# Kernel optimization log

Measured on AMD Instinct MI355X. Metric: run time of the kernel, lower is better.

Reference implementation:

```python
import jax, jax.numpy as jnp
import numpy as np
import math

N_HEADS = 16  # matches init_kwargs n_heads


def setup_inputs() -> dict:
    key = jax.random.key(0)
    k1, k2, k3 = jax.random.split(key, 3)
    B, S, D = 8, 1024, 1024
    x = jax.random.normal(k1, (B, S, D), dtype=jnp.float32)
    Wc = jax.random.normal(k2, (D, 3 * D), dtype=jnp.float32) * 0.02
    bc = jnp.zeros((3 * D,), dtype=jnp.float32)
    Wo = jax.random.normal(k3, (D, D), dtype=jnp.float32) * 0.02
    bo = jnp.zeros((D,), dtype=jnp.float32)
    return {"x": x, "Wc": Wc, "bc": bc, "Wo": Wo, "bo": bo}


def reference(x, Wc, bc, Wo, bo):
    B, S, D = x.shape
    H = N_HEADS
    hd = D // H
    qkv = x @ Wc + bc                         # [B,S,3D]
    q, k, v = jnp.split(qkv, 3, axis=2)
    q = q.reshape(B, S, H, hd)
    k = k.reshape(B, S, H, hd)
    v = v.reshape(B, S, H, hd)
    # NOTE: source scales by sqrt(d_size), not sqrt(head_dim)
    scores = jnp.einsum("bqhd,bkhd->bhqk", q, k) / math.sqrt(D)
    # source mask: triu(ones) kept, zeros (k < q) filled with float32 min
    # i.e. attend only to positions k >= q (anti-causal, faithful to source)
    keep = jnp.triu(jnp.ones((S, S), dtype=bool))  # [S,S]
    neg = jnp.finfo(jnp.float32).min
    scores = jnp.where(keep[None, None, :, :], scores, neg)
    attn = jax.nn.softmax(scores, axis=-1)    # [B,H,S,S]; dropout p=0 -> identity
    out = jnp.einsum("bhqk,bkhd->bqhd", attn, v)
    concat = out.reshape(B, S, D)
    return concat @ Wo + bo                   # final dropout p=0 -> identity
```

## Files before the change

### kernel.cpp

```cpp
#include <hip/hip_runtime.h>
#include <stdint.h>

typedef __attribute__((ext_vector_type(8))) short  bf16x8;
typedef __attribute__((ext_vector_type(4))) short  short4v;
typedef __attribute__((ext_vector_type(4))) float  f32x4;
typedef __attribute__((ext_vector_type(4))) float  float4v;

#define VMW(N) asm volatile("s_waitcnt vmcnt(" #N ")" ::: "memory")
#define BAR()  asm volatile("s_barrier" ::: "memory")

__device__ __forceinline__ short f2bf(float f) {
  union { float f; uint32_t u; } c; c.f = f;
  uint32_t u = c.u;
  uint32_t r = (u + 0x7FFFu + ((u >> 16) & 1u)) >> 16;
  return (short)(uint16_t)r;
}

__device__ __forceinline__ short f2bf_hw(float f) {
  return __builtin_bit_cast(short, (__bf16)f);
}

__device__ __forceinline__ void gload_lds16(const void* g, void* l) {
  __builtin_amdgcn_global_load_lds(
      (const __attribute__((address_space(1))) void*)g,
      (__attribute__((address_space(3))) void*)l, 16, 0, 0);
}

__device__ __forceinline__ void transpose_body(
    const float* __restrict__ in, short* __restrict__ out, int R, int C,
    int bx, int by, short (*tile)[65]) {
  int bc = bx * 64, br = by * 64;
  int tc = threadIdx.x & 63, tr = threadIdx.x >> 6;
#pragma unroll
  for (int i = 0; i < 64; i += 4)
    tile[tc][tr + i] = f2bf(in[(size_t)(br + tr + i) * C + bc + tc]);
  __syncthreads();
#pragma unroll
  for (int i = 0; i < 64; i += 4)
    out[(size_t)(bc + tr + i) * R + br + tc] = tile[tr + i][tc];
}

__global__ __launch_bounds__(256) void k_prep(
    const float* __restrict__ x, short* __restrict__ xb, int n4,
    const float* __restrict__ Wc, short* __restrict__ wct,
    const float* __restrict__ Wo, short* __restrict__ wot) {
  __shared__ short tile[64][65];
  const int id = blockIdx.x;
  if (id < 1024) {
    const int stride = 1024 * 256;
    for (int i = id * 256 + threadIdx.x; i < n4; i += stride) {
      float4v v = *(const float4v*)(x + (size_t)i * 4);
      short4v o;
      o.x = f2bf(v.x); o.y = f2bf(v.y); o.z = f2bf(v.z); o.w = f2bf(v.w);
      *(short4v*)(xb + (size_t)i * 4) = o;
    }
  } else if (id < 1024 + 768) {
    int t = id - 1024;
    transpose_body(Wc, wct, 1024, 3072, t % 48, t / 48, tile);
  } else {
    int t = id - 1792;
    transpose_body(Wo, wot, 1024, 1024, t & 15, t >> 4, tile);
  }
}

template <bool F32OUT>
__global__ __launch_bounds__(256) void k_gemm2(
    const short* __restrict__ A, const short* __restrict__ BT,
    const float* __restrict__ bias, void* __restrict__ Cout,
    int M, int N, int K, int nbn) {
  __shared__ short SM[2][2][2][128][32];
  const int tid = threadIdx.x;
  const int w = tid >> 6, l = tid & 63;
  const int fr = l & 15, fg = l >> 4;
  const int wm = w >> 1, wn = w & 1;

  const int q8 = gridDim.x >> 3;
  const int wg = (blockIdx.x & 7) * q8 + (blockIdx.x >> 3);
  const int bm = wg / nbn, bn = wg % nbn;
  const size_t brow = (size_t)bm << 7;
  const int bcol = bn << 7;

  const int NT = K >> 6;

  const int srow = l >> 2;
  const int soct = (l & 3) ^ ((l >> 3) & 3);
  const short* aG = A + (brow + srow) * (size_t)K + soct * 8;
  const short* bG = BT + ((size_t)(bcol + srow)) * K + soct * 8;
  const int slot8 = ((fg ^ ((fr >> 1) & 3)) << 3);

  f32x4 acc[4][4] = {};

#pragma unroll
  for (int s = 0; s < 6; ++s) {
    const int t = s >> 2, tau = s & 3, buf = t & 1, mat = tau & 1, kh = tau >> 1;
    const int kbase = t * 64 + kh * 32;
    const short* g0 = (mat ? bG : aG) + kbase;
#pragma unroll
    for (int j = 0; j < 2; ++j) {
      const int r0 = (w * 2 + j) * 16;
      gload_lds16(g0 + (size_t)r0 * K, (char*)&SM[buf][mat][kh][r0][0]);
    }
  }
  VMW(8);
  BAR();

  int sidx = 6;
  for (int t = 0; t < NT; ++t) {
    const int buf = t & 1;
#pragma unroll
    for (int p = 0; p < 2; ++p) {
      const int kh = p;
#pragma unroll
      for (int s = 0; s < 2; ++s) {
        if (sidx < NT * 4) {
          const int ts = sidx >> 2, tau = sidx & 3;
          const int sb = ts & 1, mat = tau & 1, skh = tau >> 1;
          const int kbase = ts * 64 + skh * 32;
          const short* g0 = (mat ? bG : aG) + kbase;
#pragma unroll
          for (int j = 0; j < 2; ++j) {
            const int r0 = (w * 2 + j) * 16;
            gload_lds16(g0 + (size_t)r0 * K, (char*)&SM[sb][mat][skh][r0][0]);
          }
          ++sidx;
        }
      }
      bf16x8 af[4], bf[4];
#pragma unroll
      for (int m = 0; m < 4; ++m)
        af[m] = *(const bf16x8*)&SM[buf][0][kh][wm * 64 + m * 16 + fr][slot8];
#pragma unroll
      for (int n = 0; n < 4; ++n)
        bf[n] = *(const bf16x8*)&SM[buf][1][kh][wn * 64 + n * 16 + fr][slot8];
      BAR();
      __builtin_amdgcn_s_setprio(1);
#pragma unroll
      for (int m = 0; m < 4; ++m)
#pragma unroll
        for (int n = 0; n < 4; ++n)
          acc[m][n] = __builtin_amdgcn_mfma_f32_16x16x32_bf16(
              af[m], bf[n], acc[m][n], 0, 0, 0);
      __builtin_amdgcn_s_setprio(0);
      if (!(t == NT - 1 && p == 1)) {
        if (t == NT - 1 && p == 0) { VMW(0); }
        else if (t == NT - 2 && p == 1) { VMW(4); }
        else { VMW(8); }
        BAR();
      }
    }
  }

#pragma unroll
  for (int n = 0; n < 4; ++n) {
    const int col = bcol + wn * 64 + n * 16 + fr;
    const float bv = bias[col];
#pragma unroll
    for (int i = 0; i < 4; ++i) {
      const size_t row = brow + (size_t)(wm * 64 + i * 16 + fg * 4);
#pragma unroll
      for (int r = 0; r < 4; ++r) {
        const float v = acc[i][n][r] + bv;
        if (F32OUT)
          ((float*)Cout)[(row + r) * (size_t)N + col] = v;
        else
          ((short*)Cout)[(row + r) * (size_t)N + col] = f2bf(v);
      }
    }
  }
}

__global__ __launch_bounds__(256) void k_attn(
    const short* __restrict__ qkv, short* __restrict__ outc, int Bn, int S) {
  __shared__ short Ks[128][64];
  __shared__ short Vt[64][136];

  const int tid = threadIdx.x;
  const int w = tid >> 6, l = tid & 63;
  const int fr = l & 15, fg = l >> 4;

  const int tq = blockIdx.x >> 7;
  const int bh = blockIdx.x & 127;
  const int h = bh & 15, b = bh >> 4;
  const int q0 = tq << 6;

  const size_t rowbase = (size_t)b * S;
  const int qcol = q0 + w * 16 + fr;

  bf16x8 qf[2];
  {
    const short* qp = qkv + (rowbase + qcol) * 3072 + h * 64 + fg * 8;
    qf[0] = *(const bf16x8*)qp;
    qf[1] = *(const bf16x8*)(qp + 32);
    const float C2 = 0.04508422f;
#pragma unroll
    for (int j = 0; j < 8; ++j) {
      union { float f; uint32_t u; } ca, cb;
      ca.u = ((uint32_t)(uint16_t)qf[0][j]) << 16;
      cb.u = ((uint32_t)(uint16_t)qf[1][j]) << 16;
      qf[0][j] = f2bf_hw(ca.f * C2);
      qf[1][j] = f2bf_hw(cb.f * C2);
    }
  }

  f32x4 o[4] = {};
  float lacc = 0.0f;

  const short* Kbase = qkv + rowbase * 3072 + 1024 + h * 64;
  const short* Vbase = qkv + rowbase * 3072 + 2048 + h * 64;

  const int r8 = l >> 3, slot = l & 7;
  const int vdb = (tid >> 4) << 2;

#define STAGE_K(c)                                                             \
  {                                                                            \
    const int k0s = (c) << 7;                                                  \
    _Pragma("unroll") for (int j = 0; j < 4; ++j) {                            \
      int ch = w * 4 + j;                                                      \
      int row = ch * 8 + r8;                                                   \
      int d = (slot ^ (row & 7)) << 3;                                         \
      gload_lds16(Kbase + (size_t)(k0s + row) * 3072 + d,                      \
                  (char*)&Ks[0][0] + ch * 1024);                               \
    }                                                                          \
  }
#define LOAD_V(c)                                                              \
  {                                                                            \
    const int k0s = (c) << 7;                                                  \
    _Pragma("unroll") for (int kh = 0; kh < 2; ++kh) {                         \
      int kb = ((tid & 15) << 2) + (kh << 6);                                  \
      const short* vp = Vbase + (size_t)(k0s + kb) * 3072 + vdb;               \
      vr[kh][0] = *(const short4v*)(vp);                                       \
      vr[kh][1] = *(const short4v*)(vp + 3072);                                \
      vr[kh][2] = *(const short4v*)(vp + 2 * 3072);                            \
      vr[kh][3] = *(const short4v*)(vp + 3 * 3072);                            \
    }                                                                          \
  }

  const int c0 = tq >> 1;
  short4v vr[2][4];
  STAGE_K(c0);
  LOAD_V(c0);

  for (int c = c0; c < 8; ++c) {
    const int k0 = c << 7;
    VMW(0);
    __syncthreads();

#pragma unroll
    for (int kh = 0; kh < 2; ++kh) {
      int kb = ((tid & 15) << 2) + (kh << 6);
      short4v t0 = {vr[kh][0].x, vr[kh][1].x, vr[kh][2].x, vr[kh][3].x};
      short4v t1 = {vr[kh][0].y, vr[kh][1].y, vr[kh][2].y, vr[kh][3].y};
      short4v t2 = {vr[kh][0].z, vr[kh][1].z, vr[kh][2].z, vr[kh][3].z};
      short4v t3 = {vr[kh][0].w, vr[kh][1].w, vr[kh][2].w, vr[kh][3].w};
      *(short4v*)&Vt[vdb + 0][kb] = t0;
      *(short4v*)&Vt[vdb + 1][kb] = t1;
      *(short4v*)&Vt[vdb + 2][kb] = t2;
      *(short4v*)&Vt[vdb + 3][kb] = t3;
    }

    f32x4 st[8];
#pragma unroll
    for (int kb = 0; kb < 8; ++kb) {
      f32x4 z = {0.f, 0.f, 0.f, 0.f};
      int row = kb * 16 + fr;
      int sw = row & 7;
      bf16x8 kf0 = *(const bf16x8*)&Ks[row][(fg ^ sw) << 3];
      bf16x8 kf1 = *(const bf16x8*)&Ks[row][((4 + fg) ^ sw) << 3];
      z = __builtin_amdgcn_mfma_f32_16x16x32_bf16(kf0, qf[0], z, 0, 0, 0);
      z = __builtin_amdgcn_mfma_f32_16x16x32_bf16(kf1, qf[1], z, 0, 0, 0);
      st[kb] = z;
    }

    if (c + 1 < 8) LOAD_V(c + 1);

    const bool masked = (c == c0);
#pragma unroll
    for (int kb = 0; kb < 8; ++kb)
#pragma unroll
      for (int r = 0; r < 4; ++r) {
        float e = exp2f(st[kb][r]);
        if (masked) {
          int kg = k0 + kb * 16 + fg * 4 + r;
          e = (kg < qcol) ? 0.0f : e;
        }
        st[kb][r] = e;
        lacc += e;
      }

    __syncthreads();

    if (c + 1 < 8) STAGE_K(c + 1);

#pragma unroll
    for (int kb2 = 0; kb2 < 4; ++kb2) {
      bf16x8 pa = {f2bf_hw(st[2 * kb2][0]),     f2bf_hw(st[2 * kb2][1]),
                   f2bf_hw(st[2 * kb2][2]),     f2bf_hw(st[2 * kb2][3]),
                   f2bf_hw(st[2 * kb2 + 1][0]), f2bf_hw(st[2 * kb2 + 1][1]),
                   f2bf_hw(st[2 * kb2 + 1][2]), f2bf_hw(st[2 * kb2 + 1][3])};
#pragma unroll
      for (int f = 0; f < 4; ++f) {
        short4v v0 = *(const short4v*)&Vt[f * 16 + fr][kb2 * 32 + fg * 4];
        short4v v1 = *(const short4v*)&Vt[f * 16 + fr][kb2 * 32 + 16 + fg * 4];
        bf16x8 vb = {v0.x, v0.y, v0.z, v0.w, v1.x, v1.y, v1.z, v1.w};
        o[f] = __builtin_amdgcn_mfma_f32_16x16x32_bf16(pa, vb, o[f], 0, 0, 0);
      }
    }
  }
#undef STAGE_K
#undef LOAD_V

  lacc += __shfl_xor(lacc, 16, 64);
  lacc += __shfl_xor(lacc, 32, 64);
#pragma unroll
  for (int r = 0; r < 4; ++r) {
    float denom = __shfl(lacc, fg * 4 + r, 64);
    float inv = 1.0f / denom;
    size_t orow = rowbase + (size_t)(q0 + w * 16 + fg * 4 + r);
    short* op = outc + orow * 1024 + h * 64 + fr;
#pragma unroll
    for (int f = 0; f < 4; ++f) op[f * 16] = f2bf(o[f][r] * inv);
  }
}

extern "C" void kernel_launch(void* const* d_in, const int* in_sizes, int n_in,
                              void* d_out, int out_size, void* d_ws,
                              size_t ws_size, hipStream_t stream) {
  const float* x = (const float*)d_in[0];
  const float* Wc = (const float*)d_in[1];
  const float* bc = (const float*)d_in[2];
  const float* Wo = (const float*)d_in[3];
  const float* bo = (const float*)d_in[4];
  float* out = (float*)d_out;

  const int Bn = 8, S = 1024, D = 1024;
  const int M = Bn * S;

  char* ws = (char*)d_ws;
  short* xb  = (short*)(ws);
  short* wct = (short*)(ws + (size_t)16 * 1024 * 1024);
  short* wot = (short*)(ws + (size_t)22 * 1024 * 1024);
  short* qkv = (short*)(ws + (size_t)24 * 1024 * 1024);
  short* cat = (short*)(ws + (size_t)72 * 1024 * 1024);

  k_prep<<<2048, 256, 0, stream>>>(x, xb, M * D / 4, Wc, wct, Wo, wot);
  k_gemm2<false><<<(M / 128) * (3 * D / 128), 256, 0, stream>>>(
      xb, wct, bc, qkv, M, 3 * D, D, 3 * D / 128);
  k_attn<<<16 * 128, 256, 0, stream>>>(qkv, cat, Bn, S);
  k_gemm2<true><<<(M / 128) * (D / 128), 256, 0, stream>>>(
      cat, wot, bo, out, M, D, D, D / 128);
}
```

Before: 159.0 us.

## Restructure GEMM pipeline into triple-buffered 32-wide K stages

Replaces the double-buffered 64-wide K tile loop (split into two 32-wide halves with fine-grained staged loads) with a triple-buffered ring of 32-wide K stages prefetched two steps ahead. Each iteration uses one barrier before issuing the next prefetch and computing, and shared memory drops from 4 to 3 half-tiles. This simplifies the issue schedule and sync pattern, but leaves less compute per barrier and changes how load latency overlaps with MFMA work.

```diff
diff --git a/kernel.cpp b/kernel.cpp
--- a/kernel.cpp
+++ b/kernel.cpp
@@ -68,7 +68,7 @@
     const short* __restrict__ A, const short* __restrict__ BT,
     const float* __restrict__ bias, void* __restrict__ Cout,
     int M, int N, int K, int nbn) {
-  __shared__ short SM[2][2][2][128][32];
+  __shared__ short SM[3][2][128][32];
   const int tid = threadIdx.x;
   const int w = tid >> 6, l = tid & 63;
   const int fr = l & 15, fg = l >> 4;
@@ -80,7 +80,7 @@
   const size_t brow = (size_t)bm << 7;
   const int bcol = bn << 7;
 
-  const int NT = K >> 6;
+  const int NT = K >> 5;
 
   const int srow = l >> 2;
   const int soct = (l & 3) ^ ((l >> 3) & 3);
@@ -90,65 +90,46 @@
 
   f32x4 acc[4][4] = {};
 
-#pragma unroll
-  for (int s = 0; s < 6; ++s) {
-    const int t = s >> 2, tau = s & 3, buf = t & 1, mat = tau & 1, kh = tau >> 1;
-    const int kbase = t * 64 + kh * 32;
-    const short* g0 = (mat ? bG : aG) + kbase;
-#pragma unroll
-    for (int j = 0; j < 2; ++j) {
-      const int r0 = (w * 2 + j) * 16;
-      gload_lds16(g0 + (size_t)r0 * K, (char*)&SM[buf][mat][kh][r0][0]);
-    }
-  }
-  VMW(8);
+#define STAGE_T(bufv, kt)                                                      \
+  {                                                                            \
+    _Pragma("unroll") for (int j = 0; j < 2; ++j) {                            \
+      const int r0 = (w * 2 + j) * 16;                                         \
+      gload_lds16(aG + (size_t)r0 * K + (kt)*32,                               \
+                  (char*)&SM[bufv][0][r0][0]);                                 \
+      gload_lds16(bG + (size_t)r0 * K + (kt)*32,                               \
+                  (char*)&SM[bufv][1][r0][0]);                                 \
+    }                                                                          \
+  }
+
+  STAGE_T(0, 0);
+  STAGE_T(1, 1);
+  VMW(4);
   BAR();
 
-  int sidx = 6;
   for (int t = 0; t < NT; ++t) {
-    const int buf = t & 1;
-#pragma unroll
-    for (int p = 0; p < 2; ++p) {
-      const int kh = p;
-#pragma unroll
-      for (int s = 0; s < 2; ++s) {
-        if (sidx < NT * 4) {
-          const int ts = sidx >> 2, tau = sidx & 3;
-          const int sb = ts & 1, mat = tau & 1, skh = tau >> 1;
-          const int kbase = ts * 64 + skh * 32;
-          const short* g0 = (mat ? bG : aG) + kbase;
-#pragma unroll
-          for (int j = 0; j < 2; ++j) {
-            const int r0 = (w * 2 + j) * 16;
-            gload_lds16(g0 + (size_t)r0 * K, (char*)&SM[sb][mat][skh][r0][0]);
-          }
-          ++sidx;
-        }
-      }
-      bf16x8 af[4], bf[4];
-#pragma unroll
-      for (int m = 0; m < 4; ++m)
-        af[m] = *(const bf16x8*)&SM[buf][0][kh][wm * 64 + m * 16 + fr][slot8];
+    const int buf = t % 3;
+    if (t > 0) {
+      if (t == NT - 1) { VMW(0); } else { VMW(4); }
+      BAR();
+    }
+    if (t + 2 < NT) STAGE_T((t + 2) % 3, t + 2);
+    bf16x8 af[4], bf[4];
+#pragma unroll
+    for (int m = 0; m < 4; ++m)
+      af[m] = *(const bf16x8*)&SM[buf][0][wm * 64 + m * 16 + fr][slot8];
+#pragma unroll
+    for (int n = 0; n < 4; ++n)
+      bf[n] = *(const bf16x8*)&SM[buf][1][wn * 64 + n * 16 + fr][slot8];
+    __builtin_amdgcn_s_setprio(1);
+#pragma unroll
+    for (int m = 0; m < 4; ++m)
 #pragma unroll
       for (int n = 0; n < 4; ++n)
-        bf[n] = *(const bf16x8*)&SM[buf][1][kh][wn * 64 + n * 16 + fr][slot8];
-      BAR();
-      __builtin_amdgcn_s_setprio(1);
-#pragma unroll
-      for (int m = 0; m < 4; ++m)
-#pragma unroll
-        for (int n = 0; n < 4; ++n)
-          acc[m][n] = __builtin_amdgcn_mfma_f32_16x16x32_bf16(
-              af[m], bf[n], acc[m][n], 0, 0, 0);
-      __builtin_amdgcn_s_setprio(0);
-      if (!(t == NT - 1 && p == 1)) {
-        if (t == NT - 1 && p == 0) { VMW(0); }
-        else if (t == NT - 2 && p == 1) { VMW(4); }
-        else { VMW(8); }
-        BAR();
-      }
-    }
-  }
+        acc[m][n] = __builtin_amdgcn_mfma_f32_16x16x32_bf16(
+            af[m], bf[n], acc[m][n], 0, 0, 0);
+    __builtin_amdgcn_s_setprio(0);
+  }
+#undef STAGE_T
 
 #pragma unroll
   for (int n = 0; n < 4; ++n) {
```

After: 159.7 us. About the same (+0.4%).

## Process two 64-row query tiles per attention block to reuse K/V loads

Applied to the files above, without the earlier changes.

Each attention block now handles 128 query rows (two 64-row tiles) instead of 64, so every K/V chunk staged in LDS serves twice as many queries and the grid is halved. This cuts global K/V traffic and the per-chunk staging and barrier overhead. In exchange each thread holds twice the accumulators and Q fragments, which raises register pressure and may lower occupancy. The second tile also processes the diagonal chunk, where about half of its work is masked out.

```diff
diff --git a/kernel.cpp b/kernel.cpp
--- a/kernel.cpp
+++ b/kernel.cpp
@@ -178,44 +178,54 @@
   const int w = tid >> 6, l = tid & 63;
   const int fr = l & 15, fg = l >> 4;
 
-  const int tq = blockIdx.x >> 7;
+  const int j = blockIdx.x >> 7;
   const int bh = blockIdx.x & 127;
   const int h = bh & 15, b = bh >> 4;
-  const int q0 = tq << 6;
+  const int q0a = j << 7;
+  const int q0b = q0a + 64;
 
   const size_t rowbase = (size_t)b * S;
-  const int qcol = q0 + w * 16 + fr;
-
-  bf16x8 qf[2];
+  const int qcola = q0a + w * 16 + fr;
+  const int qcolb = qcola + 64;
+
+  bf16x8 qfa[2], qfb[2];
   {
-    const short* qp = qkv + (rowbase + qcol) * 3072 + h * 64 + fg * 8;
-    qf[0] = *(const bf16x8*)qp;
-    qf[1] = *(const bf16x8*)(qp + 32);
     const float C2 = 0.04508422f;
-#pragma unroll
-    for (int j = 0; j < 8; ++j) {
-      union { float f; uint32_t u; } ca, cb;
-      ca.u = ((uint32_t)(uint16_t)qf[0][j]) << 16;
-      cb.u = ((uint32_t)(uint16_t)qf[1][j]) << 16;
-      qf[0][j] = f2bf_hw(ca.f * C2);
-      qf[1][j] = f2bf_hw(cb.f * C2);
-    }
-  }
-
-  f32x4 o[4] = {};
-  float lacc = 0.0f;
+    const short* qp = qkv + (rowbase + qcola) * 3072 + h * 64 + fg * 8;
+    const short* qq = qp + (size_t)64 * 3072;
+    qfa[0] = *(const bf16x8*)qp;  qfa[1] = *(const bf16x8*)(qp + 32);
+    qfb[0] = *(const bf16x8*)qq;  qfb[1] = *(const bf16x8*)(qq + 32);
+#pragma unroll
+    for (int i = 0; i < 8; ++i) {
+      union { float f; uint32_t u; } c0u, c1u, c2u, c3u;
+      c0u.u = ((uint32_t)(uint16_t)qfa[0][i]) << 16;
+      c1u.u = ((uint32_t)(uint16_t)qfa[1][i]) << 16;
+      c2u.u = ((uint32_t)(uint16_t)qfb[0][i]) << 16;
+      c3u.u = ((uint32_t)(uint16_t)qfb[1][i]) << 16;
+      qfa[0][i] = f2bf_hw(c0u.f * C2);
+      qfa[1][i] = f2bf_hw(c1u.f * C2);
+      qfb[0][i] = f2bf_hw(c2u.f * C2);
+      qfb[1][i] = f2bf_hw(c3u.f * C2);
+    }
+  }
+
+  f32x4 oa[4] = {}, ob[4] = {};
+  float la = 0.0f, lb = 0.0f;
 
   const short* Kbase = qkv + rowbase * 3072 + 1024 + h * 64;
   const short* Vbase = qkv + rowbase * 3072 + 2048 + h * 64;
 
   const int r8 = l >> 3, slot = l & 7;
   const int vdb = (tid >> 4) << 2;
+  const int c0 = j;
+
+  short4v vr[2][4];
 
 #define STAGE_K(c)                                                             \
   {                                                                            \
     const int k0s = (c) << 7;                                                  \
-    _Pragma("unroll") for (int j = 0; j < 4; ++j) {                            \
-      int ch = w * 4 + j;                                                      \
+    _Pragma("unroll") for (int jj = 0; jj < 4; ++jj) {                         \
+      int ch = w * 4 + jj;                                                     \
       int row = ch * 8 + r8;                                                   \
       int d = (slot ^ (row & 7)) << 3;                                         \
       gload_lds16(Kbase + (size_t)(k0s + row) * 3072 + d,                      \
@@ -235,13 +245,59 @@
     }                                                                          \
   }
 
-  const int c0 = tq >> 1;
-  short4v vr[2][4];
+  auto qksm = [&](const bf16x8* qf, int qcol, float& lac, bf16x8* pa, int c) {
+    f32x4 st[8];
+#pragma unroll
+    for (int kb = 0; kb < 8; ++kb) {
+      f32x4 z = {0.f, 0.f, 0.f, 0.f};
+      int row = kb * 16 + fr;
+      int sw = row & 7;
+      bf16x8 kf0 = *(const bf16x8*)&Ks[row][(fg ^ sw) << 3];
+      bf16x8 kf1 = *(const bf16x8*)&Ks[row][((4 + fg) ^ sw) << 3];
+      z = __builtin_amdgcn_mfma_f32_16x16x32_bf16(kf0, qf[0], z, 0, 0, 0);
+      z = __builtin_amdgcn_mfma_f32_16x16x32_bf16(kf1, qf[1], z, 0, 0, 0);
+      st[kb] = z;
+    }
+    const bool masked = (c == c0);
+    const int k0m = c << 7;
+#pragma unroll
+    for (int kb = 0; kb < 8; ++kb)
+#pragma unroll
+      for (int r = 0; r < 4; ++r) {
+        float e = exp2f(st[kb][r]);
+        if (masked) {
+          int kg = k0m + kb * 16 + fg * 4 + r;
+          e = (kg < qcol) ? 0.0f : e;
+        }
+        st[kb][r] = e;
+        lac += e;
+      }
+#pragma unroll
+    for (int kb2 = 0; kb2 < 4; ++kb2) {
+      bf16x8 t = {f2bf_hw(st[2 * kb2][0]),     f2bf_hw(st[2 * kb2][1]),
+                  f2bf_hw(st[2 * kb2][2]),     f2bf_hw(st[2 * kb2][3]),
+                  f2bf_hw(st[2 * kb2 + 1][0]), f2bf_hw(st[2 * kb2 + 1][1]),
+                  f2bf_hw(st[2 * kb2 + 1][2]), f2bf_hw(st[2 * kb2 + 1][3])};
+      pa[kb2] = t;
+    }
+  };
+  auto pv = [&](const bf16x8* pa, f32x4* o) {
+#pragma unroll
+    for (int kb2 = 0; kb2 < 4; ++kb2) {
+#pragma unroll
+      for (int f = 0; f < 4; ++f) {
+        short4v v0 = *(const short4v*)&Vt[f * 16 + fr][kb2 * 32 + fg * 4];
+        short4v v1 = *(const short4v*)&Vt[f * 16 + fr][kb2 * 32 + 16 + fg * 4];
+        bf16x8 vb = {v0.x, v0.y, v0.z, v0.w, v1.x, v1.y, v1.z, v1.w};
+        o[f] = __builtin_amdgcn_mfma_f32_16x16x32_bf16(pa[kb2], vb, o[f], 0, 0, 0);
+      }
+    }
+  };
+
   STAGE_K(c0);
   LOAD_V(c0);
 
   for (int c = c0; c < 8; ++c) {
-    const int k0 = c << 7;
     VMW(0);
     __syncthreads();
 
@@ -258,67 +314,40 @@
       *(short4v*)&Vt[vdb + 3][kb] = t3;
     }
 
-    f32x4 st[8];
-#pragma unroll
-    for (int kb = 0; kb < 8; ++kb) {
-      f32x4 z = {0.f, 0.f, 0.f, 0.f};
-      int row = kb * 16 + fr;
-      int sw = row & 7;
-      bf16x8 kf0 = *(const bf16x8*)&Ks[row][(fg ^ sw) << 3];
-      bf16x8 kf1 = *(const bf16x8*)&Ks[row][((4 + fg) ^ sw) << 3];
-      z = __builtin_amdgcn_mfma_f32_16x16x32_bf16(kf0, qf[0], z, 0, 0, 0);
-      z = __builtin_amdgcn_mfma_f32_16x16x32_bf16(kf1, qf[1], z, 0, 0, 0);
-      st[kb] = z;
-    }
+    bf16x8 pa_a[4], pa_b[4];
+    qksm(qfa, qcola, la, pa_a, c);
+    qksm(qfb, qcolb, lb, pa_b, c);
 
     if (c + 1 < 8) LOAD_V(c + 1);
 
-    const bool masked = (c == c0);
-#pragma unroll
-    for (int kb = 0; kb < 8; ++kb)
-#pragma unroll
-      for (int r = 0; r < 4; ++r) {
-        float e = exp2f(st[kb][r]);
-        if (masked) {
-          int kg = k0 + kb * 16 + fg * 4 + r;
-          e = (kg < qcol) ? 0.0f : e;
-        }
-        st[kb][r] = e;
-        lacc += e;
-      }
-
     __syncthreads();
 
     if (c + 1 < 8) STAGE_K(c + 1);
 
-#pragma unroll
-    for (int kb2 = 0; kb2 < 4; ++kb2) {
-      bf16x8 pa = {f2bf_hw(st[2 * kb2][0]),     f2bf_hw(st[2 * kb2][1]),
-                   f2bf_hw(st[2 * kb2][2]),     f2bf_hw(st[2 * kb2][3]),
-                   f2bf_hw(st[2 * kb2 + 1][0]), f2bf_hw(st[2 * kb2 + 1][1]),
-                   f2bf_hw(st[2 * kb2 + 1][2]), f2bf_hw(st[2 * kb2 + 1][3])};
-#pragma unroll
-      for (int f = 0; f < 4; ++f) {
-        short4v v0 = *(const short4v*)&Vt[f * 16 + fr][kb2 * 32 + fg * 4];
-        short4v v1 = *(const short4v*)&Vt[f * 16 + fr][kb2 * 32 + 16 + fg * 4];
-        bf16x8 vb = {v0.x, v0.y, v0.z, v0.w, v1.x, v1.y, v1.z, v1.w};
-        o[f] = __builtin_amdgcn_mfma_f32_16x16x32_bf16(pa, vb, o[f], 0, 0, 0);
-      }
-    }
+    pv(pa_a, oa);
+    pv(pa_b, ob);
   }
 #undef STAGE_K
 #undef LOAD_V
 
-  lacc += __shfl_xor(lacc, 16, 64);
-  lacc += __shfl_xor(lacc, 32, 64);
+  la += __shfl_xor(la, 16, 64);
+  la += __shfl_xor(la, 32, 64);
+  lb += __shfl_xor(lb, 16, 64);
+  lb += __shfl_xor(lb, 32, 64);
 #pragma unroll
   for (int r = 0; r < 4; ++r) {
-    float denom = __shfl(lacc, fg * 4 + r, 64);
-    float inv = 1.0f / denom;
-    size_t orow = rowbase + (size_t)(q0 + w * 16 + fg * 4 + r);
-    short* op = outc + orow * 1024 + h * 64 + fr;
-#pragma unroll
-    for (int f = 0; f < 4; ++f) op[f * 16] = f2bf(o[f][r] * inv);
+    float da = __shfl(la, fg * 4 + r, 64);
+    float db = __shfl(lb, fg * 4 + r, 64);
+    float ia = 1.0f / da, ib = 1.0f / db;
+    size_t ra = rowbase + (size_t)(q0a + w * 16 + fg * 4 + r);
+    size_t rb = ra + 64;
+    short* opa = outc + ra * 1024 + h * 64 + fr;
+    short* opb = outc + rb * 1024 + h * 64 + fr;
+#pragma unroll
+    for (int f = 0; f < 4; ++f) {
+      opa[f * 16] = f2bf(oa[f][r] * ia);
+      opb[f * 16] = f2bf(ob[f][r] * ib);
+    }
   }
 }
 
@@ -345,7 +374,7 @@
   k_prep<<<2048, 256, 0, stream>>>(x, xb, M * D / 4, Wc, wct, Wo, wot);
   k_gemm2<false><<<(M / 128) * (3 * D / 128), 256, 0, stream>>>(
       xb, wct, bc, qkv, M, 3 * D, D, 3 * D / 128);
-  k_attn<<<16 * 128, 256, 0, stream>>>(qkv, cat, Bn, S);
+  k_attn<<<8 * 128, 256, 0, stream>>>(qkv, cat, Bn, S);
   k_gemm2<true><<<(M / 128) * (D / 128), 256, 0, stream>>>(
       cat, wot, bo, out, M, D, D, D / 128);
 }
```

Result: slower. 174.0 us (+9.4%).
